# Optimization experiments

Measured on AMD Instinct MI355X. Metric: run time of the kernel, lower is better.

Reference implementation:

```python
import jax, jax.numpy as jnp
import numpy as np

B, L, S = 8, 8192, 512
DQ, DC = 256, 768
H, DH = 8, 64
INNER = H * DH


def setup_inputs() -> dict:
    key = jax.random.key(0)
    ks = jax.random.split(key, 8)
    std_q = 1.0 / np.sqrt(DQ)
    std_c = 1.0 / np.sqrt(DC)
    std_o = 1.0 / np.sqrt(INNER)
    return {
        "x": jax.random.normal(ks[0], (B, L, DQ), jnp.float32),
        "context": jax.random.normal(ks[1], (B, S, DC), jnp.float32),
        "seq_lens": jax.random.randint(ks[2], (B,), 1, L + 1, jnp.int32),
        "Wq": jax.random.normal(ks[3], (DQ, INNER), jnp.float32) * std_q,
        "Wk": jax.random.normal(ks[4], (DC, INNER), jnp.float32) * std_c,
        "Wv": jax.random.normal(ks[5], (DC, INNER), jnp.float32) * std_c,
        "Wo": jax.random.normal(ks[6], (INNER, DQ), jnp.float32) * std_o,
        "bo": jnp.zeros((DQ,), jnp.float32),
    }


def reference(x, context, seq_lens, Wq, Wk, Wv, Wo, bo):
    # x: [B, L, DQ] padded jagged voxel features; seq_lens: valid count per batch.
    # Equivalent to the per-batch SDPA loop: each batch's queries attend over
    # that batch's full (unmasked) context of S tokens.
    scale = 1.0 / np.sqrt(DH)
    q = (x @ Wq).reshape(B, L, H, DH).transpose(0, 2, 1, 3)        # [B,H,L,DH]
    k = (context @ Wk).reshape(B, S, H, DH).transpose(0, 2, 1, 3)  # [B,H,S,DH]
    v = (context @ Wv).reshape(B, S, H, DH).transpose(0, 2, 1, 3)  # [B,H,S,DH]
    scores = jnp.einsum("bhld,bhsd->bhls", q, k) * scale           # [B,H,L,S]
    attn = jax.nn.softmax(scores, axis=-1)
    out = jnp.einsum("bhls,bhsd->bhld", attn, v)                   # [B,H,L,DH]
    out = out.transpose(0, 2, 1, 3).reshape(B, L, INNER)
    out = out @ Wo + bo                                            # [B,L,DQ]
    valid = (jnp.arange(L)[None, :] < seq_lens[:, None])[..., None]
    return jnp.where(valid, out, 0.0)
```

## Files before the change

### kernel.cpp

```cpp
#include <hip/hip_runtime.h>
#include <hip/hip_bf16.h>

#define DEV __device__ __forceinline__

typedef float f32x4 __attribute__((ext_vector_type(4)));
typedef unsigned short u16x4 __attribute__((ext_vector_type(4)));
typedef unsigned short u16x8 __attribute__((ext_vector_type(8)));
typedef __bf16 bf16x8 __attribute__((ext_vector_type(8)));

DEV unsigned short f2b(float f) { __bf16 h = (__bf16)f; return __builtin_bit_cast(unsigned short, h); }
DEV bf16x8 asbf8(u16x8 v) { return __builtin_bit_cast(bf16x8, v); }

#define MFMA(a, b, c) __builtin_amdgcn_mfma_f32_16x16x32_bf16((a), (b), (c), 0, 0, 0)

constexpr float QSCALE = 0.18033688011112042f;
constexpr float MFIX = 20.0f;

__global__ __launch_bounds__(256) void convert_weights(
    const float* __restrict__ Wq, const float* __restrict__ Wk,
    const float* __restrict__ Wv, const float* __restrict__ Wo,
    unsigned short* __restrict__ WqT, unsigned short* __restrict__ WkvT,
    unsigned short* __restrict__ WoT)
{
  int i = blockIdx.x * 256 + threadIdx.x;
  if (i < 131072) {
    int n = i >> 8, k = i & 255;
    WqT[i] = f2b(Wq[k * 512 + n] * QSCALE);
  } else if (i < 131072 + 786432) {
    int j = i - 131072;
    int n = j / 768, k = j - n * 768;
    float v = (n < 512) ? Wk[k * 512 + n] : Wv[k * 512 + (n - 512)];
    WkvT[j] = f2b(v);
  } else {
    int j = i - 917504;
    int n = j >> 9, k = j & 511;
    WoT[j] = f2b(Wo[k * 256 + n]);
  }
}

template<int KDIM, int NCOLS, bool AF32, int EPI>
__global__ __launch_bounds__(256, AF32 ? 3 : 4) void proj_gemm(
    const float* __restrict__ Af, const unsigned short* __restrict__ Ab,
    const unsigned short* __restrict__ BT, const int* __restrict__ seq_lens,
    unsigned short* __restrict__ out0, unsigned short* __restrict__ out1,
    float* __restrict__ outf, const float* __restrict__ bo)
{
  constexpr int WC = NCOLS / 4;
  constexpr int NCT = WC / 16;
  constexpr int KSTEPS = KDIM / 32;
  constexpr int ASZ = AF32 ? (64 * 36 * 4) : (64 * 32 * 2);
  const int t = threadIdx.x;
  const int wid = t >> 6, lane = t & 63;
  const int q = lane & 15, g = lane >> 4;
  const int row0 = blockIdx.x * 64;
  const int wcol = blockIdx.y * NCOLS + wid * WC;

  int sl = 0;
  if (EPI == 0 || EPI == 2) {
    sl = seq_lens[row0 >> 13];
    if ((row0 & 8191) >= sl) {
      if (EPI == 2 && blockIdx.y == 0) {
        f32x4 z = {0.f, 0.f, 0.f, 0.f};
        float* o = outf + (size_t)row0 * 256;
        #pragma unroll
        for (int i = 0; i < 16; ++i)
          *(f32x4*)(o + (size_t)(i * 256 + t) * 4) = z;
      }
      return;
    }
  }

  __shared__ __align__(16) char smem[2 * ASZ];

  const int ar0 = t >> 3, akc = (t & 7) * 4;
  const int br0 = t >> 2, bkc = (t & 3) * 8;

  f32x4 acc[4][NCT];
  #pragma unroll
  for (int i = 0; i < 4; ++i)
    #pragma unroll
    for (int j = 0; j < NCT; ++j) acc[i][j] = {0.f, 0.f, 0.f, 0.f};

  f32x4 a0, a1;
  u16x8 ab;
  if (AF32) {
    a0 = *(const f32x4*)(Af + (size_t)(row0 + ar0) * KDIM + akc);
    a1 = *(const f32x4*)(Af + (size_t)(row0 + 32 + ar0) * KDIM + akc);
    float* Lf = (float*)smem;
    *(f32x4*)(Lf + ar0 * 36 + akc) = a0;
    *(f32x4*)(Lf + (32 + ar0) * 36 + akc) = a1;
  } else {
    ab = *(const u16x8*)(Ab + (size_t)(row0 + br0) * KDIM + bkc);
    *(u16x8*)((unsigned short*)smem + br0 * 32 + bkc) = ab;
  }
  bf16x8 bcur[NCT];
  #pragma unroll
  for (int ct = 0; ct < NCT; ++ct)
    bcur[ct] = asbf8(*(const u16x8*)(BT + (size_t)(wcol + ct * 16 + q) * KDIM + g * 8));
  __syncthreads();

  #pragma unroll 2
  for (int st = 0; st < KSTEPS; ++st) {
    const int cur = st & 1;
    const int k1 = (st + 1) * 32;

    if (st + 1 < KSTEPS) {
      if (AF32) {
        a0 = *(const f32x4*)(Af + (size_t)(row0 + ar0) * KDIM + k1 + akc);
        a1 = *(const f32x4*)(Af + (size_t)(row0 + 32 + ar0) * KDIM + k1 + akc);
      } else {
        ab = *(const u16x8*)(Ab + (size_t)(row0 + br0) * KDIM + k1 + bkc);
      }
    }
    bf16x8 bnx[NCT];
    if (st + 1 < KSTEPS) {
      #pragma unroll
      for (int ct = 0; ct < NCT; ++ct)
        bnx[ct] = asbf8(*(const u16x8*)(BT + (size_t)(wcol + ct * 16 + q) * KDIM + k1 + g * 8));
    }

    bf16x8 af[4];
    if (AF32) {
      const float* Lf = (const float*)(smem + cur * ASZ);
      #pragma unroll
      for (int rt = 0; rt < 4; ++rt) {
        const float* pp = Lf + (rt * 16 + q) * 36 + g * 8;
        f32x4 lo = *(const f32x4*)pp;
        f32x4 hi = *(const f32x4*)(pp + 4);
        u16x8 u;
        u[0] = f2b(lo[0]); u[1] = f2b(lo[1]); u[2] = f2b(lo[2]); u[3] = f2b(lo[3]);
        u[4] = f2b(hi[0]); u[5] = f2b(hi[1]); u[6] = f2b(hi[2]); u[7] = f2b(hi[3]);
        af[rt] = asbf8(u);
      }
    } else {
      const unsigned short* Lb = (const unsigned short*)(smem + cur * ASZ);
      #pragma unroll
      for (int rt = 0; rt < 4; ++rt)
        af[rt] = asbf8(*(const u16x8*)(Lb + (rt * 16 + q) * 32 + g * 8));
    }

    #pragma unroll
    for (int ct = 0; ct < NCT; ++ct)
      #pragma unroll
      for (int rt = 0; rt < 4; ++rt)
        acc[rt][ct] = MFMA(af[rt], bcur[ct], acc[rt][ct]);

    if (st + 1 < KSTEPS) {
      if (AF32) {
        float* Lf = (float*)(smem + (cur ^ 1) * ASZ);
        *(f32x4*)(Lf + ar0 * 36 + akc) = a0;
        *(f32x4*)(Lf + (32 + ar0) * 36 + akc) = a1;
      } else {
        *(u16x8*)((unsigned short*)(smem + (cur ^ 1) * ASZ) + br0 * 32 + bkc) = ab;
      }
      #pragma unroll
      for (int ct = 0; ct < NCT; ++ct) bcur[ct] = bnx[ct];
    }
    __syncthreads();
  }

  if (EPI == 0) {
    const int bb = row0 >> 13, l0 = row0 & 8191;
    #pragma unroll
    for (int ct = 0; ct < NCT; ++ct) {
      int col = wcol + ct * 16 + q;
      int hh = col >> 6, d = col & 63;
      unsigned short* o = out0 + (((size_t)bb * 8 + hh) * 8192) * 64 + d;
      #pragma unroll
      for (int rt = 0; rt < 4; ++rt)
        #pragma unroll
        for (int r = 0; r < 4; ++r) {
          int ll = l0 + rt * 16 + g * 4 + r;
          o[(size_t)ll * 64] = f2b(acc[rt][ct][r]);
        }
    }
  } else if (EPI == 1) {
    const int bb = row0 >> 9, s0 = row0 & 511;
    #pragma unroll
    for (int ct = 0; ct < NCT; ++ct) {
      int col = wcol + ct * 16 + q;
      if (col < 512) {
        int hh = col >> 6, d = col & 63;
        #pragma unroll
        for (int rt = 0; rt < 4; ++rt)
          #pragma unroll
          for (int r = 0; r < 4; ++r) {
            int s = s0 + rt * 16 + g * 4 + r;
            out0[(((size_t)bb * 8 + hh) * 512 + s) * 64 + d] = f2b(acc[rt][ct][r]);
          }
      } else {
        int c2 = col - 512, hh = c2 >> 6, d = c2 & 63;
        #pragma unroll
        for (int rt = 0; rt < 4; ++rt)
          #pragma unroll
          for (int r = 0; r < 4; ++r) {
            int s = s0 + rt * 16 + g * 4 + r;
            out1[(((size_t)bb * 8 + hh) * 64 + d) * 512 + s] = f2b(acc[rt][ct][r]);
          }
      }
    }
  } else {
    const int l0 = row0 & 8191;
    #pragma unroll
    for (int ct = 0; ct < NCT; ++ct) {
      int col = wcol + ct * 16 + q;
      float bias = bo[col];
      #pragma unroll
      for (int rt = 0; rt < 4; ++rt)
        #pragma unroll
        for (int r = 0; r < 4; ++r) {
          int ll = l0 + rt * 16 + g * 4 + r;
          float v = acc[rt][ct][r] + bias;
          outf[(size_t)(row0 + rt * 16 + g * 4 + r) * 256 + col] = (ll < sl) ? v : 0.f;
        }
    }
  }
}

__global__ __launch_bounds__(256, 4) void attn_kernel(
    const unsigned short* __restrict__ Qw, const unsigned short* __restrict__ Kw,
    const unsigned short* __restrict__ VTw, const int* __restrict__ seq_lens,
    unsigned short* __restrict__ AO)
{
  const int wid = threadIdx.x >> 6, lane = threadIdx.x & 63;
  const int q = lane & 15, g = lane >> 4;
  const int h  = blockIdx.x & 7;
  const int lb = blockIdx.x >> 3;
  const int NB = gridDim.x >> 3;

  __shared__ __align__(16) unsigned short Ks[2][32 * 64];
  __shared__ __align__(16) unsigned short Vs[2][64 * 32];

  const int krow  = (wid << 3) + (lane >> 3);
  const int kslot = (lane & 7) ^ (lane >> 3);
  const int vd    = (wid << 4) + (lane >> 2);
  const int vc    = lane & 3;
  const int vswz  = (vd >> 1) & 3;
  const int vs0   = (((2 * vc) & 3) ^ vswz) * 8 + ((vc >> 1) * 4);
  const int vs1   = (((2 * vc + 1) & 3) ^ vswz) * 8 + ((vc >> 1) * 4);
  const int vrslot = (g ^ ((q >> 1) & 3)) * 8;

  int off[9];
  off[0] = 0;
  #pragma unroll
  for (int b = 0; b < 8; ++b)
    off[b + 1] = off[b] + ((seq_lens[b] + 127) >> 7);
  const int total = off[8];

  for (int it = lb; it < total; it += NB) {
    int b = 0;
    while (it >= off[b + 1]) ++b;
    const int qbase = (it - off[b]) * 128 + wid * 32;
    const bool wactive = qbase < seq_lens[b];

    const unsigned short* Qb = Qw + (((size_t)b * 8 + h) * 8192 + qbase) * 64;
    const unsigned short* Kb = Kw + ((size_t)b * 8 + h) * (512 * 64);
    const unsigned short* Vb = VTw + ((size_t)b * 8 + h) * (64 * 512);

    bf16x8 qf[2][2];
    if (wactive) {
      #pragma unroll
      for (int qt = 0; qt < 2; ++qt)
        #pragma unroll
        for (int dc = 0; dc < 2; ++dc)
          qf[qt][dc] = asbf8(*(const u16x8*)(Qb + (qt * 16 + q) * 64 + dc * 32 + g * 8));
    }

    f32x4 acc[2][4];
    float lsum[2] = {0.f, 0.f};
    #pragma unroll
    for (int qt = 0; qt < 2; ++qt)
      #pragma unroll
      for (int dt = 0; dt < 4; ++dt) acc[qt][dt] = {0.f, 0.f, 0.f, 0.f};

    {
      u16x8 kr = *(const u16x8*)(Kb + krow * 64 + (lane & 7) * 8);
      u16x8 vr = *(const u16x8*)(Vb + vd * 512 + vc * 8);
      *(u16x8*)(&Ks[0][krow * 64 + kslot * 8]) = kr;
      u16x4 vlo, vhi;
      vlo[0] = vr[0]; vlo[1] = vr[1]; vlo[2] = vr[2]; vlo[3] = vr[3];
      vhi[0] = vr[4]; vhi[1] = vr[5]; vhi[2] = vr[6]; vhi[3] = vr[7];
      *(u16x4*)(&Vs[0][vd * 32 + vs0]) = vlo;
      *(u16x4*)(&Vs[0][vd * 32 + vs1]) = vhi;
    }
    __syncthreads();

    #pragma unroll 2
    for (int st = 0; st < 16; ++st) {
      const int cur = st & 1;
      const int scn = (st + 1) * 32;

      u16x8 kn, vn;
      if (st < 15) {
        kn = *(const u16x8*)(Kb + (scn + krow) * 64 + (lane & 7) * 8);
        vn = *(const u16x8*)(Vb + vd * 512 + scn + vc * 8);
      }

      if (wactive) {
        bf16x8 kf[2][2];
        #pragma unroll
        for (int tt = 0; tt < 2; ++tt)
          #pragma unroll
          for (int dc = 0; dc < 2; ++dc)
            kf[tt][dc] = asbf8(*(const u16x8*)(
                &Ks[cur][(tt * 16 + q) * 64 + ((dc * 4 + g) ^ (q & 7)) * 8]));

        bf16x8 va[4];
        #pragma unroll
        for (int dt = 0; dt < 4; ++dt)
          va[dt] = asbf8(*(const u16x8*)(&Vs[cur][(dt * 16 + q) * 32 + vrslot]));

        #pragma unroll
        for (int qt = 0; qt < 2; ++qt) {
          f32x4 t0 = {-MFIX, -MFIX, -MFIX, -MFIX};
          f32x4 t1 = {-MFIX, -MFIX, -MFIX, -MFIX};
          t0 = MFMA(kf[0][0], qf[qt][0], t0);
          t0 = MFMA(kf[0][1], qf[qt][1], t0);
          t1 = MFMA(kf[1][0], qf[qt][0], t1);
          t1 = MFMA(kf[1][1], qf[qt][1], t1);

          float p0 = __builtin_amdgcn_exp2f(t0[0]);
          float p1 = __builtin_amdgcn_exp2f(t0[1]);
          float p2 = __builtin_amdgcn_exp2f(t0[2]);
          float p3 = __builtin_amdgcn_exp2f(t0[3]);
          float p4 = __builtin_amdgcn_exp2f(t1[0]);
          float p5 = __builtin_amdgcn_exp2f(t1[1]);
          float p6 = __builtin_amdgcn_exp2f(t1[2]);
          float p7 = __builtin_amdgcn_exp2f(t1[3]);
          lsum[qt] += ((p0 + p1) + (p2 + p3)) + ((p4 + p5) + (p6 + p7));

          u16x8 pu;
          pu[0] = f2b(p0); pu[1] = f2b(p1); pu[2] = f2b(p2); pu[3] = f2b(p3);
          pu[4] = f2b(p4); pu[5] = f2b(p5); pu[6] = f2b(p6); pu[7] = f2b(p7);
          bf16x8 pb = asbf8(pu);

          #pragma unroll
          for (int dt = 0; dt < 4; ++dt)
            acc[qt][dt] = MFMA(va[dt], pb, acc[qt][dt]);
        }
      }

      if (st < 15) {
        const int nb = cur ^ 1;
        *(u16x8*)(&Ks[nb][krow * 64 + kslot * 8]) = kn;
        u16x4 vlo, vhi;
        vlo[0] = vn[0]; vlo[1] = vn[1]; vlo[2] = vn[2]; vlo[3] = vn[3];
        vhi[0] = vn[4]; vhi[1] = vn[5]; vhi[2] = vn[6]; vhi[3] = vn[7];
        *(u16x4*)(&Vs[nb][vd * 32 + vs0]) = vlo;
        *(u16x4*)(&Vs[nb][vd * 32 + vs1]) = vhi;
      }
      __syncthreads();
    }

    if (wactive) {
      #pragma unroll
      for (int qt = 0; qt < 2; ++qt) {
        float lt = lsum[qt];
        lt += __shfl_xor(lt, 16);
        lt += __shfl_xor(lt, 32);
        float inv = __builtin_amdgcn_rcpf(lt);
        size_t ro = ((size_t)b * 8192 + qbase + qt * 16 + q) * 512 + h * 64;
        #pragma unroll
        for (int dt = 0; dt < 4; ++dt) {
          u16x4 o;
          o[0] = f2b(acc[qt][dt][0] * inv);
          o[1] = f2b(acc[qt][dt][1] * inv);
          o[2] = f2b(acc[qt][dt][2] * inv);
          o[3] = f2b(acc[qt][dt][3] * inv);
          *(u16x4*)(AO + ro + dt * 16 + g * 4) = o;
        }
      }
    }
  }
}

extern "C" void kernel_launch(void* const* d_in, const int* in_sizes, int n_in,
                              void* d_out, int out_size, void* d_ws, size_t ws_size,
                              hipStream_t stream) {
  const float* x   = (const float*)d_in[0];
  const float* ctx = (const float*)d_in[1];
  const int*   seq = (const int*)d_in[2];
  const float* Wq  = (const float*)d_in[3];
  const float* Wk  = (const float*)d_in[4];
  const float* Wv  = (const float*)d_in[5];
  const float* Wo  = (const float*)d_in[6];
  const float* bo  = (const float*)d_in[7];
  float* Y = (float*)d_out;

  unsigned short* ws = (unsigned short*)d_ws;
  unsigned short* WqT  = ws;
  unsigned short* WkvT = WqT + 131072;
  unsigned short* WoT  = WkvT + 786432;
  unsigned short* Qws  = WoT + 131072;
  unsigned short* Kws  = Qws + 33554432;
  unsigned short* VTws = Kws + 2097152;
  unsigned short* AOws = VTws + 2097152;

  convert_weights<<<4096, 256, 0, stream>>>(Wq, Wk, Wv, Wo, WqT, WkvT, WoT);

  proj_gemm<256, 256, true, 0><<<dim3(1024, 2), 256, 0, stream>>>(
      x, nullptr, WqT, seq, Qws, nullptr, nullptr, nullptr);

  proj_gemm<768, 256, true, 1><<<dim3(64, 4), 256, 0, stream>>>(
      ctx, nullptr, WkvT, seq, Kws, VTws, nullptr, nullptr);

  attn_kernel<<<2048, 256, 0, stream>>>(Qws, Kws, VTws, seq, AOws);

  proj_gemm<512, 128, false, 2><<<dim3(1024, 2), 256, 0, stream>>>(
      nullptr, AOws, WoT, seq, nullptr, nullptr, Y, bo);
}
```

Measured before the change: 165.2 us.

## Launch one attention block per tile and stage 64-key chunks per barrier

Replaces the persistent grid-stride loop over packed valid tiles with a full grid of 4096 blocks, one per (batch, 128-query tile, head), where blocks past seq_len exit immediately. It also doubles the shared-memory stage so each iteration loads and processes 64 keys, halving the number of __syncthreads. Occupancy is lowered to 3 blocks per SM to allow the larger buffers and extra registers. The aim is less scheduling imbalance and fewer barriers, at the cost of launching many empty blocks and using more LDS per block.

```diff
diff --git a/kernel.cpp b/kernel.cpp
--- a/kernel.cpp
+++ b/kernel.cpp
@@ -217,19 +217,25 @@
   }
 }
 
-__global__ __launch_bounds__(256, 4) void attn_kernel(
+__global__ __launch_bounds__(256, 3) void attn_kernel(
     const unsigned short* __restrict__ Qw, const unsigned short* __restrict__ Kw,
     const unsigned short* __restrict__ VTw, const int* __restrict__ seq_lens,
     unsigned short* __restrict__ AO)
 {
+  const int bid = blockIdx.x;
+  const int h = bid & 7;
+  const int tile = (bid >> 3) & 63;
+  const int b = bid >> 9;
+
+  const int sl = seq_lens[b];
+  const int qbase0 = tile * 128;
+  if (qbase0 >= sl) return;
+
   const int wid = threadIdx.x >> 6, lane = threadIdx.x & 63;
   const int q = lane & 15, g = lane >> 4;
-  const int h  = blockIdx.x & 7;
-  const int lb = blockIdx.x >> 3;
-  const int NB = gridDim.x >> 3;
-
-  __shared__ __align__(16) unsigned short Ks[2][32 * 64];
-  __shared__ __align__(16) unsigned short Vs[2][64 * 32];
+
+  __shared__ __align__(16) unsigned short Ks[2][2][32 * 64];
+  __shared__ __align__(16) unsigned short Vs[2][2][64 * 32];
 
   const int krow  = (wid << 3) + (lane >> 3);
   const int kslot = (lane & 7) ^ (lane >> 3);
@@ -240,75 +246,72 @@
   const int vs1   = (((2 * vc + 1) & 3) ^ vswz) * 8 + ((vc >> 1) * 4);
   const int vrslot = (g ^ ((q >> 1) & 3)) * 8;
 
-  int off[9];
-  off[0] = 0;
+  const int qbase = qbase0 + wid * 32;
+  const bool wactive = qbase < sl;
+
+  const unsigned short* Qb = Qw + (((size_t)b * 8 + h) * 8192 + qbase) * 64;
+  const unsigned short* Kb = Kw + ((size_t)b * 8 + h) * (512 * 64);
+  const unsigned short* Vb = VTw + ((size_t)b * 8 + h) * (64 * 512);
+
+  bf16x8 qf[2][2];
+  if (wactive) {
+    #pragma unroll
+    for (int qt = 0; qt < 2; ++qt)
+      #pragma unroll
+      for (int dc = 0; dc < 2; ++dc)
+        qf[qt][dc] = asbf8(*(const u16x8*)(Qb + (qt * 16 + q) * 64 + dc * 32 + g * 8));
+  }
+
+  f32x4 acc[2][4];
+  float lsum[2] = {0.f, 0.f};
   #pragma unroll
-  for (int b = 0; b < 8; ++b)
-    off[b + 1] = off[b] + ((seq_lens[b] + 127) >> 7);
-  const int total = off[8];
-
-  for (int it = lb; it < total; it += NB) {
-    int b = 0;
-    while (it >= off[b + 1]) ++b;
-    const int qbase = (it - off[b]) * 128 + wid * 32;
-    const bool wactive = qbase < seq_lens[b];
-
-    const unsigned short* Qb = Qw + (((size_t)b * 8 + h) * 8192 + qbase) * 64;
-    const unsigned short* Kb = Kw + ((size_t)b * 8 + h) * (512 * 64);
-    const unsigned short* Vb = VTw + ((size_t)b * 8 + h) * (64 * 512);
-
-    bf16x8 qf[2][2];
-    if (wactive) {
-      #pragma unroll
-      for (int qt = 0; qt < 2; ++qt)
-        #pragma unroll
-        for (int dc = 0; dc < 2; ++dc)
-          qf[qt][dc] = asbf8(*(const u16x8*)(Qb + (qt * 16 + q) * 64 + dc * 32 + g * 8));
-    }
-
-    f32x4 acc[2][4];
-    float lsum[2] = {0.f, 0.f};
-    #pragma unroll
-    for (int qt = 0; qt < 2; ++qt)
-      #pragma unroll
-      for (int dt = 0; dt < 4; ++dt) acc[qt][dt] = {0.f, 0.f, 0.f, 0.f};
-
-    {
-      u16x8 kr = *(const u16x8*)(Kb + krow * 64 + (lane & 7) * 8);
-      u16x8 vr = *(const u16x8*)(Vb + vd * 512 + vc * 8);
-      *(u16x8*)(&Ks[0][krow * 64 + kslot * 8]) = kr;
+  for (int qt = 0; qt < 2; ++qt)
+    #pragma unroll
+    for (int dt = 0; dt < 4; ++dt) acc[qt][dt] = {0.f, 0.f, 0.f, 0.f};
+
+  {
+    #pragma unroll
+    for (int s2 = 0; s2 < 2; ++s2) {
+      u16x8 kr = *(const u16x8*)(Kb + (s2 * 32 + krow) * 64 + (lane & 7) * 8);
+      u16x8 vr = *(const u16x8*)(Vb + vd * 512 + s2 * 32 + vc * 8);
+      *(u16x8*)(&Ks[0][s2][krow * 64 + kslot * 8]) = kr;
       u16x4 vlo, vhi;
       vlo[0] = vr[0]; vlo[1] = vr[1]; vlo[2] = vr[2]; vlo[3] = vr[3];
       vhi[0] = vr[4]; vhi[1] = vr[5]; vhi[2] = vr[6]; vhi[3] = vr[7];
-      *(u16x4*)(&Vs[0][vd * 32 + vs0]) = vlo;
-      *(u16x4*)(&Vs[0][vd * 32 + vs1]) = vhi;
-    }
-    __syncthreads();
-
-    #pragma unroll 2
-    for (int st = 0; st < 16; ++st) {
-      const int cur = st & 1;
-      const int scn = (st + 1) * 32;
-
-      u16x8 kn, vn;
-      if (st < 15) {
-        kn = *(const u16x8*)(Kb + (scn + krow) * 64 + (lane & 7) * 8);
-        vn = *(const u16x8*)(Vb + vd * 512 + scn + vc * 8);
-      }
-
-      if (wactive) {
+      *(u16x4*)(&Vs[0][s2][vd * 32 + vs0]) = vlo;
+      *(u16x4*)(&Vs[0][s2][vd * 32 + vs1]) = vhi;
+    }
+  }
+  __syncthreads();
+
+  for (int st = 0; st < 8; ++st) {
+    const int cur = st & 1;
+    const int scn = (st + 1) * 64;
+
+    u16x8 kn[2], vn[2];
+    if (st < 7) {
+      #pragma unroll
+      for (int s2 = 0; s2 < 2; ++s2) {
+        kn[s2] = *(const u16x8*)(Kb + (scn + s2 * 32 + krow) * 64 + (lane & 7) * 8);
+        vn[s2] = *(const u16x8*)(Vb + vd * 512 + scn + s2 * 32 + vc * 8);
+      }
+    }
+
+    if (wactive) {
+      #pragma unroll
+      for (int c = 0; c < 2; ++c) {
         bf16x8 kf[2][2];
         #pragma unroll
         for (int tt = 0; tt < 2; ++tt)
           #pragma unroll
           for (int dc = 0; dc < 2; ++dc)
             kf[tt][dc] = asbf8(*(const u16x8*)(
-                &Ks[cur][(tt * 16 + q) * 64 + ((dc * 4 + g) ^ (q & 7)) * 8]));
+                &Ks[cur][c][(tt * 16 + q) * 64 + ((dc * 4 + g) ^ (q & 7)) * 8]));
 
         bf16x8 va[4];
         #pragma unroll
         for (int dt = 0; dt < 4; ++dt)
-          va[dt] = asbf8(*(const u16x8*)(&Vs[cur][(dt * 16 + q) * 32 + vrslot]));
+          va[dt] = asbf8(*(const u16x8*)(&Vs[cur][c][(dt * 16 + q) * 32 + vrslot]));
 
         #pragma unroll
         for (int qt = 0; qt < 2; ++qt) {
@@ -339,36 +342,39 @@
             acc[qt][dt] = MFMA(va[dt], pb, acc[qt][dt]);
         }
       }
-
-      if (st < 15) {
-        const int nb = cur ^ 1;
-        *(u16x8*)(&Ks[nb][krow * 64 + kslot * 8]) = kn;
+    }
+
+    if (st < 7) {
+      const int nb = cur ^ 1;
+      #pragma unroll
+      for (int s2 = 0; s2 < 2; ++s2) {
+        *(u16x8*)(&Ks[nb][s2][krow * 64 + kslot * 8]) = kn[s2];
         u16x4 vlo, vhi;
-        vlo[0] = vn[0]; vlo[1] = vn[1]; vlo[2] = vn[2]; vlo[3] = vn[3];
-        vhi[0] = vn[4]; vhi[1] = vn[5]; vhi[2] = vn[6]; vhi[3] = vn[7];
-        *(u16x4*)(&Vs[nb][vd * 32 + vs0]) = vlo;
-        *(u16x4*)(&Vs[nb][vd * 32 + vs1]) = vhi;
-      }
-      __syncthreads();
-    }
-
-    if (wactive) {
-      #pragma unroll
-      for (int qt = 0; qt < 2; ++qt) {
-        float lt = lsum[qt];
-        lt += __shfl_xor(lt, 16);
-        lt += __shfl_xor(lt, 32);
-        float inv = __builtin_amdgcn_rcpf(lt);
-        size_t ro = ((size_t)b * 8192 + qbase + qt * 16 + q) * 512 + h * 64;
-        #pragma unroll
-        for (int dt = 0; dt < 4; ++dt) {
-          u16x4 o;
-          o[0] = f2b(acc[qt][dt][0] * inv);
-          o[1] = f2b(acc[qt][dt][1] * inv);
-          o[2] = f2b(acc[qt][dt][2] * inv);
-          o[3] = f2b(acc[qt][dt][3] * inv);
-          *(u16x4*)(AO + ro + dt * 16 + g * 4) = o;
-        }
+        vlo[0] = vn[s2][0]; vlo[1] = vn[s2][1]; vlo[2] = vn[s2][2]; vlo[3] = vn[s2][3];
+        vhi[0] = vn[s2][4]; vhi[1] = vn[s2][5]; vhi[2] = vn[s2][6]; vhi[3] = vn[s2][7];
+        *(u16x4*)(&Vs[nb][s2][vd * 32 + vs0]) = vlo;
+        *(u16x4*)(&Vs[nb][s2][vd * 32 + vs1]) = vhi;
+      }
+    }
+    __syncthreads();
+  }
+
+  if (wactive) {
+    #pragma unroll
+    for (int qt = 0; qt < 2; ++qt) {
+      float lt = lsum[qt];
+      lt += __shfl_xor(lt, 16);
+      lt += __shfl_xor(lt, 32);
+      float inv = __builtin_amdgcn_rcpf(lt);
+      size_t ro = ((size_t)b * 8192 + qbase + qt * 16 + q) * 512 + h * 64;
+      #pragma unroll
+      for (int dt = 0; dt < 4; ++dt) {
+        u16x4 o;
+        o[0] = f2b(acc[qt][dt][0] * inv);
+        o[1] = f2b(acc[qt][dt][1] * inv);
+        o[2] = f2b(acc[qt][dt][2] * inv);
+        o[3] = f2b(acc[qt][dt][3] * inv);
+        *(u16x4*)(AO + ro + dt * 16 + g * 4) = o;
       }
     }
   }
@@ -404,7 +410,7 @@
   proj_gemm<768, 256, true, 1><<<dim3(64, 4), 256, 0, stream>>>(
       ctx, nullptr, WkvT, seq, Kws, VTws, nullptr, nullptr);
 
-  attn_kernel<<<2048, 256, 0, stream>>>(Qws, Kws, VTws, seq, AOws);
+  attn_kernel<<<4096, 256, 0, stream>>>(Qws, Kws, VTws, seq, AOws);
 
   proj_gemm<512, 128, false, 2><<<dim3(1024, 2), 256, 0, stream>>>(
       nullptr, AOws, WoT, seq, nullptr, nullptr, Y, bo);
```

Measured after the change: 156.3 us. 1.06x faster.
